# Performance work log

Hardware: AMD Instinct MI355X
Metric: run time of the kernel (lower is better)

The kernel has to match this reference:

```python
import jax, jax.numpy as jnp
import numpy as np

N_NODES = 100000
N_EDGES = 600000
N_GRAPHS = 64


def _segment_mean(x, seg_ids, num_segments):
    s = jax.ops.segment_sum(x, seg_ids, num_segments=num_segments)
    cnt = jax.ops.segment_sum(jnp.ones((x.shape[0],), x.dtype), seg_ids, num_segments=num_segments)
    return s / jnp.maximum(cnt, 1.0)[:, None]


def _sage_conv(x, src, dst, W_l, W_r, b):
    # PyG SAGEConv (mean aggr): out = lin_l(mean_{j->i} x_j) + lin_r(x_i)
    mean_nb = _segment_mean(x[src], dst, x.shape[0])  # [N, d_in]
    return mean_nb @ W_l.T + x @ W_r.T + b


def setup_inputs() -> dict:
    key = jax.random.key(0)
    ks = jax.random.split(key, 16)
    bert_cls = jax.random.normal(ks[0], (N_GRAPHS, 768), jnp.float32)
    node_x = jax.random.normal(ks[1], (N_NODES, 128), jnp.float32)
    edge_index = jax.random.randint(ks[2], (2, N_EDGES), 0, N_NODES, jnp.int64 if jax.config.jax_enable_x64 else jnp.int32)
    batch_ids = jnp.sort(jax.random.randint(ks[3], (N_NODES,), 0, N_GRAPHS))
    s = 0.05
    return {
        'bert_cls': bert_cls,
        'node_x': node_x,
        'edge_index': edge_index,
        'batch_ids': batch_ids,
        'W_adapt': jax.random.normal(ks[4], (64, 768), jnp.float32) * s,
        'b_adapt': jnp.zeros((64,), jnp.float32),
        'W1l': jax.random.normal(ks[5], (64, 128), jnp.float32) * s,
        'W1r': jax.random.normal(ks[6], (64, 128), jnp.float32) * s,
        'b1': jnp.zeros((64,), jnp.float32),
        'W2l': jax.random.normal(ks[7], (16, 64), jnp.float32) * s,
        'W2r': jax.random.normal(ks[8], (16, 64), jnp.float32) * s,
        'b2': jnp.zeros((16,), jnp.float32),
        'Wm': jax.random.normal(ks[9], (16, 16), jnp.float32) * s,
        'bm': jnp.zeros((16,), jnp.float32),
    }


def reference(bert_cls, node_x, edge_index, batch_ids,
              W_adapt, b_adapt, W1l, W1r, b1, W2l, W2r, b2, Wm, bm):
    # pooled BERT CLS -> adaptive linear (forward() applies no relu here)
    last_state = bert_cls @ W_adapt.T + b_adapt  # [bs, 64]

    src, dst = edge_index[0], edge_index[1]
    h = jax.nn.relu(_sage_conv(node_x, src, dst, W1l, W1r, b1))  # [N, 64]
    h = _sage_conv(h, src, dst, W2l, W2r, b2)                    # [N, 16]

    graph_emb = _segment_mean(h, batch_ids, N_GRAPHS)            # [bs, 16]
    graph_emb = graph_emb @ Wm.T + bm

    return jnp.concatenate([last_state, graph_emb], axis=-1)     # [bs, 80]
```

## Files before the change

kernel.cpp:

```cpp
#include <hip/hip_runtime.h>

#define N_NODES 100000
#define N_EDGES 600000
#define N_GRAPHS 64


__global__ void k_count(const int* __restrict__ dst, int* __restrict__ deg) {
    int e = blockIdx.x * 256 + threadIdx.x;
    if (e < N_EDGES) atomicAdd(&deg[dst[e]], 1);
}

__global__ void k_scan1(const int* __restrict__ deg, int* __restrict__ offs,
                        int* __restrict__ bsums) {
    __shared__ int s[256];
    int t = threadIdx.x, b = blockIdx.x;
    int base = b * 1024 + t * 4;
    int v0 = (base + 0 < N_NODES) ? deg[base + 0] : 0;
    int v1 = (base + 1 < N_NODES) ? deg[base + 1] : 0;
    int v2 = (base + 2 < N_NODES) ? deg[base + 2] : 0;
    int v3 = (base + 3 < N_NODES) ? deg[base + 3] : 0;
    int tsum = v0 + v1 + v2 + v3;
    s[t] = tsum;
    __syncthreads();
    for (int o = 1; o < 256; o <<= 1) {
        int x = (t >= o) ? s[t - o] : 0;
        __syncthreads();
        s[t] += x;
        __syncthreads();
    }
    int p = s[t] - tsum;
    if (base + 0 < N_NODES) offs[base + 0] = p;
    p += v0;
    if (base + 1 < N_NODES) offs[base + 1] = p;
    p += v1;
    if (base + 2 < N_NODES) offs[base + 2] = p;
    p += v2;
    if (base + 3 < N_NODES) offs[base + 3] = p;
    if (t == 255) bsums[b] = s[255];
}

__global__ void k_scan2(const int* __restrict__ bsums, int* __restrict__ boff) {
    __shared__ int s[128];
    int t = threadIdx.x;
    int nb = (N_NODES + 1023) / 1024;
    int v = (t < nb) ? bsums[t] : 0;
    s[t] = v;
    __syncthreads();
    for (int o = 1; o < 128; o <<= 1) {
        int x = (t >= o) ? s[t - o] : 0;
        __syncthreads();
        s[t] += x;
        __syncthreads();
    }
    boff[t] = s[t] - v;
}

__global__ void k_scan3(int* __restrict__ offs, const int* __restrict__ boff,
                        int* __restrict__ cursor) {
    int i = blockIdx.x * 256 + threadIdx.x;
    if (i < N_NODES) {
        int v = offs[i] + boff[i >> 10];
        offs[i] = v;
        cursor[i] = v;
    }
}

__global__ void k_fill(const int* __restrict__ src, const int* __restrict__ dst,
                       int* __restrict__ cursor, int* __restrict__ ssrc) {
    int e = blockIdx.x * 256 + threadIdx.x;
    if (e < N_EDGES) {
        int d = dst[e];
        int pos = atomicAdd(&cursor[d], 1);
        ssrc[pos] = src[e];
    }
}

__global__ void k_prepack(const float* __restrict__ W1l, const float* __restrict__ W1r,
                          float2* __restrict__ Wc) {
    int i = blockIdx.x * 256 + threadIdx.x;
    if (i < 128 * 64) {
        int k = i >> 6, d = i & 63;
        Wc[i] = make_float2(W1l[d * 128 + k], W1r[d * 128 + k]);
    }
}


__launch_bounds__(256)
__global__ void k_layer1(const float* __restrict__ x, const int* __restrict__ ssrc,
                         const int* __restrict__ offs, const int* __restrict__ deg,
                         const float2* __restrict__ Wc, const float* __restrict__ b1,
                         float* __restrict__ h1) {
    __shared__ float2 S[4][8][128];
    int tid = threadIdx.x, wave = tid >> 6, lane = tid & 63;
    float bias = b1[lane];
    const float2* x2 = (const float2*)x;
    int gw = blockIdx.x * 4 + wave;
    int nw = gridDim.x * 4;

    for (int base = gw * 8; base < N_NODES; base += nw * 8) {
#pragma unroll 1
        for (int j = 0; j < 8; ++j) {
            int node = base + j;
            int o  = __builtin_amdgcn_readfirstlane(offs[node]);
            int dg = __builtin_amdgcn_readfirstlane(deg[node]);
            float ax0 = 0.f, ay0 = 0.f, ax1 = 0.f, ay1 = 0.f;
            float ax2 = 0.f, ay2 = 0.f, ax3 = 0.f, ay3 = 0.f;
            int last = dg - 1;
            for (int u = 0; u < dg; u += 4) {
                int n0 = ssrc[o + u];
                int n1 = ssrc[o + min(u + 1, last)];
                int n2 = ssrc[o + min(u + 2, last)];
                int n3 = ssrc[o + min(u + 3, last)];
                float2 v0 = x2[n0 * 64 + lane];
                float2 v1 = x2[n1 * 64 + lane];
                float2 v2 = x2[n2 * 64 + lane];
                float2 v3 = x2[n3 * 64 + lane];
                float m1 = (u + 1 < dg) ? 1.f : 0.f;
                float m2 = (u + 2 < dg) ? 1.f : 0.f;
                float m3 = (u + 3 < dg) ? 1.f : 0.f;
                ax0 += v0.x;               ay0 += v0.y;
                ax1 = fmaf(v1.x, m1, ax1); ay1 = fmaf(v1.y, m1, ay1);
                ax2 = fmaf(v2.x, m2, ax2); ay2 = fmaf(v2.y, m2, ay2);
                ax3 = fmaf(v3.x, m3, ax3); ay3 = fmaf(v3.y, m3, ay3);
            }
            float inv = 1.f / (float)max(dg, 1);
            float ax = (ax0 + ax1) + (ax2 + ax3);
            float ay = (ay0 + ay1) + (ay2 + ay3);
            float2 xi = x2[node * 64 + lane];
            S[wave][j][2 * lane]     = make_float2(ax * inv, xi.x);
            S[wave][j][2 * lane + 1] = make_float2(ay * inv, xi.y);
        }
        float a0 = bias, a1 = bias, a2 = bias, a3 = bias;
        float a4 = bias, a5 = bias, a6 = bias, a7 = bias;
#pragma unroll 4
        for (int k = 0; k < 128; ++k) {
            float2 w = Wc[k * 64 + lane];
            float2 s0 = S[wave][0][k]; a0 += w.x * s0.x + w.y * s0.y;
            float2 s1 = S[wave][1][k]; a1 += w.x * s1.x + w.y * s1.y;
            float2 s2 = S[wave][2][k]; a2 += w.x * s2.x + w.y * s2.y;
            float2 s3 = S[wave][3][k]; a3 += w.x * s3.x + w.y * s3.y;
            float2 s4 = S[wave][4][k]; a4 += w.x * s4.x + w.y * s4.y;
            float2 s5 = S[wave][5][k]; a5 += w.x * s5.x + w.y * s5.y;
            float2 s6 = S[wave][6][k]; a6 += w.x * s6.x + w.y * s6.y;
            float2 s7 = S[wave][7][k]; a7 += w.x * s7.x + w.y * s7.y;
        }
        h1[(base + 0) * 64 + lane] = fmaxf(a0, 0.f);
        h1[(base + 1) * 64 + lane] = fmaxf(a1, 0.f);
        h1[(base + 2) * 64 + lane] = fmaxf(a2, 0.f);
        h1[(base + 3) * 64 + lane] = fmaxf(a3, 0.f);
        h1[(base + 4) * 64 + lane] = fmaxf(a4, 0.f);
        h1[(base + 5) * 64 + lane] = fmaxf(a5, 0.f);
        h1[(base + 6) * 64 + lane] = fmaxf(a6, 0.f);
        h1[(base + 7) * 64 + lane] = fmaxf(a7, 0.f);
    }
}


__launch_bounds__(256)
__global__ void k_layer2(const float* __restrict__ h1, const int* __restrict__ ssrc,
                         const int* __restrict__ offs, const int* __restrict__ deg,
                         const int* __restrict__ batch,
                         const float* __restrict__ W2l, const float* __restrict__ W2r,
                         const float* __restrict__ b2,
                         float* __restrict__ gsum, float* __restrict__ gcnt) {
    __shared__ float2 Wc[64 * 16];
    __shared__ float2 S[4][8][64];
    __shared__ float bins[N_GRAPHS][17];
    int tid = threadIdx.x;
    for (int i = tid; i < 64 * 16; i += 256) {
        int k = i >> 4, d = i & 15;
        Wc[i] = make_float2(W2l[d * 64 + k], W2r[d * 64 + k]);
    }
    for (int i = tid; i < N_GRAPHS * 17; i += 256) ((float*)bins)[i] = 0.f;
    __syncthreads();

    int wave = tid >> 6, lane = tid & 63;
    int d = lane & 15, jq = lane >> 4;
    float bias = b2[d];

    int chunk = (N_NODES + gridDim.x - 1) / gridDim.x;
    int cs = blockIdx.x * chunk;
    int ce = min(N_NODES, cs + chunk);

    for (int base = cs + wave * 8; base < ce; base += 32) {
        int cnt = min(8, ce - base);
        for (int j = 0; j < cnt; ++j) {
            int node = base + j;
            int o  = __builtin_amdgcn_readfirstlane(offs[node]);
            int dg = __builtin_amdgcn_readfirstlane(deg[node]);
            float a0 = 0.f, a1 = 0.f, a2 = 0.f, a3 = 0.f;
            int last = dg - 1;
            for (int u = 0; u < dg; u += 4) {
                int n0 = ssrc[o + u];
                int n1 = ssrc[o + min(u + 1, last)];
                int n2 = ssrc[o + min(u + 2, last)];
                int n3 = ssrc[o + min(u + 3, last)];
                float v0 = h1[n0 * 64 + lane];
                float v1 = h1[n1 * 64 + lane];
                float v2 = h1[n2 * 64 + lane];
                float v3 = h1[n3 * 64 + lane];
                float m1 = (u + 1 < dg) ? 1.f : 0.f;
                float m2 = (u + 2 < dg) ? 1.f : 0.f;
                float m3 = (u + 3 < dg) ? 1.f : 0.f;
                a0 += v0;
                a1 = fmaf(v1, m1, a1);
                a2 = fmaf(v2, m2, a2);
                a3 = fmaf(v3, m3, a3);
            }
            float inv = 1.f / (float)max(dg, 1);
            S[wave][j][lane] = make_float2(((a0 + a1) + (a2 + a3)) * inv,
                                           h1[node * 64 + lane]);
        }
#pragma unroll
        for (int p = 0; p < 2; ++p) {
            int j = p * 4 + jq;
            float a = bias;
#pragma unroll 8
            for (int k = 0; k < 64; ++k) {
                float2 w = Wc[k * 16 + d];
                float2 s = S[wave][j][k];
                a += w.x * s.x + w.y * s.y;
            }
            if (j < cnt) {
                int g = batch[base + j];
                atomicAdd(&bins[g][d], a);
                if (d == 0) atomicAdd(&bins[g][16], 1.f);
            }
        }
    }
    __syncthreads();
    for (int i = tid; i < N_GRAPHS * 17; i += 256) {
        int g = i / 17, c = i - g * 17;
        float v = bins[g][c];
        if (v != 0.f) {
            if (c < 16) atomicAdd(&gsum[g * 16 + c], v);
            else        atomicAdd(&gcnt[g], v);
        }
    }
}


__global__ void k_final(const float* __restrict__ bert, const float* __restrict__ Wad,
                        const float* __restrict__ bad, const float* __restrict__ Wm,
                        const float* __restrict__ bm, const float* __restrict__ gsum,
                        const float* __restrict__ gcnt, float* __restrict__ out) {
    int g = blockIdx.x;
    int t = threadIdx.x;
    if (t < 64) {
        const float4* br = (const float4*)(bert + g * 768);
        const float4* wr = (const float4*)(Wad + t * 768);
        float acc = bad[t];
#pragma unroll 8
        for (int k = 0; k < 192; ++k) {
            float4 bv = br[k], wv = wr[k];
            acc += bv.x * wv.x + bv.y * wv.y + bv.z * wv.z + bv.w * wv.w;
        }
        out[g * 80 + t] = acc;
    } else if (t < 80) {
        int j = t - 64;
        float ic = 1.f / fmaxf(gcnt[g], 1.f);
        float acc = bm[j];
#pragma unroll
        for (int k = 0; k < 16; ++k) acc += Wm[j * 16 + k] * gsum[g * 16 + k] * ic;
        out[g * 80 + t] = acc;
    }
}

extern "C" void kernel_launch(void* const* d_in, const int* in_sizes, int n_in,
                              void* d_out, int out_size, void* d_ws, size_t ws_size,
                              hipStream_t stream) {
    const float* bert   = (const float*)d_in[0];
    const float* node_x = (const float*)d_in[1];
    const int*   edge   = (const int*)d_in[2];
    const int*   batch  = (const int*)d_in[3];
    const float* Wad    = (const float*)d_in[4];
    const float* bad    = (const float*)d_in[5];
    const float* W1l    = (const float*)d_in[6];
    const float* W1r    = (const float*)d_in[7];
    const float* b1     = (const float*)d_in[8];
    const float* W2l    = (const float*)d_in[9];
    const float* W2r    = (const float*)d_in[10];
    const float* b2     = (const float*)d_in[11];
    const float* Wm     = (const float*)d_in[12];
    const float* bm     = (const float*)d_in[13];
    float* out = (float*)d_out;

    const int* src = edge;
    const int* dst = edge + N_EDGES;

    char* ws = (char*)d_ws;
    int*    deg    = (int*)(ws);
    int*    offs   = (int*)(ws + 400000);
    int*    cursor = (int*)(ws + 800000);
    int*    bsums  = (int*)(ws + 1200000);
    int*    boff   = (int*)(ws + 1200512);
    int*    ssrc   = (int*)(ws + 1201024);
    float*  h1     = (float*)(ws + 3601024);
    float2* Wc1    = (float2*)(ws + 29201024);
    float*  gsum   = (float*)(ws + 29266560);
    float*  gcnt   = (float*)(ws + 29270656);

    hipMemsetAsync(deg, 0, 400000, stream);
    hipMemsetAsync(gsum, 0, 4096 + 256, stream);

    k_count<<<(N_EDGES + 255) / 256, 256, 0, stream>>>(dst, deg);
    k_scan1<<<(N_NODES + 1023) / 1024, 256, 0, stream>>>(deg, offs, bsums);
    k_scan2<<<1, 128, 0, stream>>>(bsums, boff);
    k_scan3<<<(N_NODES + 255) / 256, 256, 0, stream>>>(offs, boff, cursor);
    k_fill<<<(N_EDGES + 255) / 256, 256, 0, stream>>>(src, dst, cursor, ssrc);
    k_prepack<<<32, 256, 0, stream>>>(W1l, W1r, Wc1);

    k_layer1<<<1024, 256, 0, stream>>>(node_x, ssrc, offs, deg, Wc1, b1, h1);
    k_layer2<<<1024, 256, 0, stream>>>(h1, ssrc, offs, deg, batch, W2l, W2r, b2, gsum, gcnt);
    k_final<<<N_GRAPHS, 128, 0, stream>>>(bert, Wad, bad, Wm, bm, gsum, gcnt, out);
}
```

Measured before the change: 365.0 us.

## Restructure SAGE layers into 64-node tiles with node-per-lane GEMM and separate pooling

Both layer kernels now gather 64 nodes per block into a swizzled shared tile, then run the dense projection with one node per lane and each wave owning a slice of output dims. Weights are read as wave-uniform values, likely scalar loads, instead of per-lane. Layer 2 writes h2 to global memory and a new k_pool kernel does the per-graph mean pooling, replacing the in-kernel atomics. The goal is to cut redundant LDS and weight traffic in the GEMM phase. The cost is an extra kernel launch, an h2 round trip, and block-wide syncs between gather and compute.

After: 460.9 us. 26.3% more time.

```diff
diff --git a/kernel.cpp b/kernel.cpp
--- a/kernel.cpp
+++ b/kernel.cpp
@@ -75,12 +75,23 @@
     }
 }
 
-__global__ void k_prepack(const float* __restrict__ W1l, const float* __restrict__ W1r,
-                          float2* __restrict__ Wc) {
+__global__ void k_prepack1(const float* __restrict__ W1l, const float* __restrict__ W1r,
+                           float2* __restrict__ Wsc) {
     int i = blockIdx.x * 256 + threadIdx.x;
     if (i < 128 * 64) {
-        int k = i >> 6, d = i & 63;
-        Wc[i] = make_float2(W1l[d * 128 + k], W1r[d * 128 + k]);
+        int m = i >> 6, d = i & 63;
+        Wsc[i] = (m < 64) ? make_float2(W1l[d * 128 + 2 * m], W1l[d * 128 + 2 * m + 1])
+                          : make_float2(W1r[d * 128 + 2 * (m - 64)], W1r[d * 128 + 2 * (m - 64) + 1]);
+    }
+}
+
+__global__ void k_prepack2(const float* __restrict__ W2l, const float* __restrict__ W2r,
+                           float2* __restrict__ Wsc) {
+    int i = blockIdx.x * 256 + threadIdx.x;
+    if (i < 64 * 16) {
+        int m = i >> 4, d = i & 15;
+        Wsc[i] = (m < 32) ? make_float2(W2l[d * 64 + 2 * m], W2l[d * 64 + 2 * m + 1])
+                          : make_float2(W2r[d * 64 + 2 * (m - 32)], W2r[d * 64 + 2 * (m - 32) + 1]);
     }
 }
 
@@ -88,70 +99,77 @@
 __launch_bounds__(256)
 __global__ void k_layer1(const float* __restrict__ x, const int* __restrict__ ssrc,
                          const int* __restrict__ offs, const int* __restrict__ deg,
-                         const float2* __restrict__ Wc, const float* __restrict__ b1,
+                         const float2* __restrict__ Wsc, const float* __restrict__ b1,
                          float* __restrict__ h1) {
-    __shared__ float2 S[4][8][128];
-    int tid = threadIdx.x, wave = tid >> 6, lane = tid & 63;
-    float bias = b1[lane];
+    __shared__ float2 S[64 * 128];
+    int tid = threadIdx.x;
+    int wave = __builtin_amdgcn_readfirstlane(tid >> 6);
+    int lane = tid & 63;
     const float2* x2 = (const float2*)x;
-    int gw = blockIdx.x * 4 + wave;
-    int nw = gridDim.x * 4;
-
-    for (int base = gw * 8; base < N_NODES; base += nw * 8) {
-#pragma unroll 1
-        for (int j = 0; j < 8; ++j) {
-            int node = base + j;
-            int o  = __builtin_amdgcn_readfirstlane(offs[node]);
-            int dg = __builtin_amdgcn_readfirstlane(deg[node]);
-            float ax0 = 0.f, ay0 = 0.f, ax1 = 0.f, ay1 = 0.f;
-            float ax2 = 0.f, ay2 = 0.f, ax3 = 0.f, ay3 = 0.f;
-            int last = dg - 1;
-            for (int u = 0; u < dg; u += 4) {
-                int n0 = ssrc[o + u];
-                int n1 = ssrc[o + min(u + 1, last)];
-                int n2 = ssrc[o + min(u + 2, last)];
-                int n3 = ssrc[o + min(u + 3, last)];
-                float2 v0 = x2[n0 * 64 + lane];
-                float2 v1 = x2[n1 * 64 + lane];
-                float2 v2 = x2[n2 * 64 + lane];
-                float2 v3 = x2[n3 * 64 + lane];
-                float m1 = (u + 1 < dg) ? 1.f : 0.f;
-                float m2 = (u + 2 < dg) ? 1.f : 0.f;
-                float m3 = (u + 3 < dg) ? 1.f : 0.f;
-                ax0 += v0.x;               ay0 += v0.y;
-                ax1 = fmaf(v1.x, m1, ax1); ay1 = fmaf(v1.y, m1, ay1);
-                ax2 = fmaf(v2.x, m2, ax2); ay2 = fmaf(v2.y, m2, ay2);
-                ax3 = fmaf(v3.x, m3, ax3); ay3 = fmaf(v3.y, m3, ay3);
-            }
-            float inv = 1.f / (float)max(dg, 1);
-            float ax = (ax0 + ax1) + (ax2 + ax3);
-            float ay = (ay0 + ay1) + (ay2 + ay3);
-            float2 xi = x2[node * 64 + lane];
-            S[wave][j][2 * lane]     = make_float2(ax * inv, xi.x);
-            S[wave][j][2 * lane + 1] = make_float2(ay * inv, xi.y);
-        }
-        float a0 = bias, a1 = bias, a2 = bias, a3 = bias;
-        float a4 = bias, a5 = bias, a6 = bias, a7 = bias;
+
+    int nTiles = (N_NODES + 63) / 64;
+    for (int tile = blockIdx.x; tile < nTiles; tile += gridDim.x) {
+        int tbase = tile * 64;
+        for (int j = wave * 16; j < wave * 16 + 16; ++j) {
+            int node = tbase + j;
+            if (node < N_NODES) {
+                int o  = __builtin_amdgcn_readfirstlane(offs[node]);
+                int dg = __builtin_amdgcn_readfirstlane(deg[node]);
+                float ax0 = 0.f, ay0 = 0.f, ax1 = 0.f, ay1 = 0.f;
+                float ax2 = 0.f, ay2 = 0.f, ax3 = 0.f, ay3 = 0.f;
+                int last = dg - 1;
+                for (int u = 0; u < dg; u += 4) {
+                    int n0 = ssrc[o + u];
+                    int n1 = ssrc[o + min(u + 1, last)];
+                    int n2 = ssrc[o + min(u + 2, last)];
+                    int n3 = ssrc[o + min(u + 3, last)];
+                    float2 v0 = x2[n0 * 64 + lane];
+                    float2 v1 = x2[n1 * 64 + lane];
+                    float2 v2 = x2[n2 * 64 + lane];
+                    float2 v3 = x2[n3 * 64 + lane];
+                    float m1 = (u + 1 < dg) ? 1.f : 0.f;
+                    float m2 = (u + 2 < dg) ? 1.f : 0.f;
+                    float m3 = (u + 3 < dg) ? 1.f : 0.f;
+                    ax0 += v0.x;               ay0 += v0.y;
+                    ax1 = fmaf(v1.x, m1, ax1); ay1 = fmaf(v1.y, m1, ay1);
+                    ax2 = fmaf(v2.x, m2, ax2); ay2 = fmaf(v2.y, m2, ay2);
+                    ax3 = fmaf(v3.x, m3, ax3); ay3 = fmaf(v3.y, m3, ay3);
+                }
+                float inv = 1.f / (float)max(dg, 1);
+                float2 xi = x2[node * 64 + lane];
+                int sw = lane ^ (j & 15);
+                S[j * 128 + sw]      = make_float2(((ax0 + ax1) + (ax2 + ax3)) * inv,
+                                                   ((ay0 + ay1) + (ay2 + ay3)) * inv);
+                S[j * 128 + 64 + sw] = make_float2(xi.x, xi.y);
+            }
+        }
+        __syncthreads();
+        {
+            int n = lane;
+            int node = tbase + n;
+            int dbase = wave * 16;
+            float acc[16];
+#pragma unroll
+            for (int dd = 0; dd < 16; ++dd) acc[dd] = b1[dbase + dd];
+            int swz = n & 15;
+            const float2* Sn = S + n * 128;
 #pragma unroll 4
-        for (int k = 0; k < 128; ++k) {
-            float2 w = Wc[k * 64 + lane];
-            float2 s0 = S[wave][0][k]; a0 += w.x * s0.x + w.y * s0.y;
-            float2 s1 = S[wave][1][k]; a1 += w.x * s1.x + w.y * s1.y;
-            float2 s2 = S[wave][2][k]; a2 += w.x * s2.x + w.y * s2.y;
-            float2 s3 = S[wave][3][k]; a3 += w.x * s3.x + w.y * s3.y;
-            float2 s4 = S[wave][4][k]; a4 += w.x * s4.x + w.y * s4.y;
-            float2 s5 = S[wave][5][k]; a5 += w.x * s5.x + w.y * s5.y;
-            float2 s6 = S[wave][6][k]; a6 += w.x * s6.x + w.y * s6.y;
-            float2 s7 = S[wave][7][k]; a7 += w.x * s7.x + w.y * s7.y;
-        }
-        h1[(base + 0) * 64 + lane] = fmaxf(a0, 0.f);
-        h1[(base + 1) * 64 + lane] = fmaxf(a1, 0.f);
-        h1[(base + 2) * 64 + lane] = fmaxf(a2, 0.f);
-        h1[(base + 3) * 64 + lane] = fmaxf(a3, 0.f);
-        h1[(base + 4) * 64 + lane] = fmaxf(a4, 0.f);
-        h1[(base + 5) * 64 + lane] = fmaxf(a5, 0.f);
-        h1[(base + 6) * 64 + lane] = fmaxf(a6, 0.f);
-        h1[(base + 7) * 64 + lane] = fmaxf(a7, 0.f);
+            for (int m = 0; m < 128; ++m) {
+                float2 s = Sn[m ^ swz];
+                const float2* Wm = Wsc + m * 64 + dbase;
+#pragma unroll
+                for (int dd = 0; dd < 16; ++dd)
+                    acc[dd] = fmaf(Wm[dd].x, s.x, fmaf(Wm[dd].y, s.y, acc[dd]));
+            }
+            if (node < N_NODES) {
+                float4* dstp = (float4*)(h1 + node * 64 + dbase);
+#pragma unroll
+                for (int p = 0; p < 4; ++p)
+                    dstp[p] = make_float4(fmaxf(acc[4 * p], 0.f), fmaxf(acc[4 * p + 1], 0.f),
+                                          fmaxf(acc[4 * p + 2], 0.f), fmaxf(acc[4 * p + 3], 0.f));
+            }
+        }
+        __syncthreads();
     }
 }
 
@@ -159,77 +177,94 @@
 __launch_bounds__(256)
 __global__ void k_layer2(const float* __restrict__ h1, const int* __restrict__ ssrc,
                          const int* __restrict__ offs, const int* __restrict__ deg,
-                         const int* __restrict__ batch,
-                         const float* __restrict__ W2l, const float* __restrict__ W2r,
-                         const float* __restrict__ b2,
-                         float* __restrict__ gsum, float* __restrict__ gcnt) {
-    __shared__ float2 Wc[64 * 16];
-    __shared__ float2 S[4][8][64];
+                         const float2* __restrict__ Wsc, const float* __restrict__ b2,
+                         float* __restrict__ h2) {
+    __shared__ float S[64 * 128];
+    int tid = threadIdx.x;
+    int wave = __builtin_amdgcn_readfirstlane(tid >> 6);
+    int lane = tid & 63;
+
+    int nTiles = (N_NODES + 63) / 64;
+    for (int tile = blockIdx.x; tile < nTiles; tile += gridDim.x) {
+        int tbase = tile * 64;
+        for (int j = wave * 16; j < wave * 16 + 16; ++j) {
+            int node = tbase + j;
+            if (node < N_NODES) {
+                int o  = __builtin_amdgcn_readfirstlane(offs[node]);
+                int dg = __builtin_amdgcn_readfirstlane(deg[node]);
+                float a0 = 0.f, a1 = 0.f, a2 = 0.f, a3 = 0.f;
+                int last = dg - 1;
+                for (int u = 0; u < dg; u += 4) {
+                    int n0 = ssrc[o + u];
+                    int n1 = ssrc[o + min(u + 1, last)];
+                    int n2 = ssrc[o + min(u + 2, last)];
+                    int n3 = ssrc[o + min(u + 3, last)];
+                    float v0 = h1[n0 * 64 + lane];
+                    float v1 = h1[n1 * 64 + lane];
+                    float v2 = h1[n2 * 64 + lane];
+                    float v3 = h1[n3 * 64 + lane];
+                    float m1 = (u + 1 < dg) ? 1.f : 0.f;
+                    float m2 = (u + 2 < dg) ? 1.f : 0.f;
+                    float m3 = (u + 3 < dg) ? 1.f : 0.f;
+                    a0 += v0;
+                    a1 = fmaf(v1, m1, a1);
+                    a2 = fmaf(v2, m2, a2);
+                    a3 = fmaf(v3, m3, a3);
+                }
+                float inv = 1.f / (float)max(dg, 1);
+                float mv = ((a0 + a1) + (a2 + a3)) * inv;
+                float hv = h1[node * 64 + lane];
+                int pr = (lane >> 1) ^ (j & 15), c = lane & 1;
+                S[j * 128 + 2 * pr + c]      = mv;
+                S[j * 128 + 64 + 2 * pr + c] = hv;
+            }
+        }
+        __syncthreads();
+        {
+            int n = lane;
+            int node = tbase + n;
+            int dbase = wave * 4;
+            float acc[4];
+#pragma unroll
+            for (int dd = 0; dd < 4; ++dd) acc[dd] = b2[dbase + dd];
+            int swz = n & 15;
+            const float2* Sn = (const float2*)S + n * 64;
+#pragma unroll 4
+            for (int m = 0; m < 64; ++m) {
+                float2 s = Sn[m ^ swz];
+                const float2* Wm = Wsc + m * 16 + dbase;
+#pragma unroll
+                for (int dd = 0; dd < 4; ++dd)
+                    acc[dd] = fmaf(Wm[dd].x, s.x, fmaf(Wm[dd].y, s.y, acc[dd]));
+            }
+            if (node < N_NODES) {
+                *(float4*)(h2 + node * 16 + dbase) =
+                    make_float4(acc[0], acc[1], acc[2], acc[3]);
+            }
+        }
+        __syncthreads();
+    }
+}
+
+
+__global__ void k_pool(const float* __restrict__ h2, const int* __restrict__ batch,
+                       float* __restrict__ gsum, float* __restrict__ gcnt) {
     __shared__ float bins[N_GRAPHS][17];
-    int tid = threadIdx.x;
-    for (int i = tid; i < 64 * 16; i += 256) {
-        int k = i >> 4, d = i & 15;
-        Wc[i] = make_float2(W2l[d * 64 + k], W2r[d * 64 + k]);
-    }
-    for (int i = tid; i < N_GRAPHS * 17; i += 256) ((float*)bins)[i] = 0.f;
+    int t = threadIdx.x;
+    for (int i = t; i < N_GRAPHS * 17; i += 256) ((float*)bins)[i] = 0.f;
     __syncthreads();
-
-    int wave = tid >> 6, lane = tid & 63;
-    int d = lane & 15, jq = lane >> 4;
-    float bias = b2[d];
-
+    int dd = t & 15, nl = t >> 4;
     int chunk = (N_NODES + gridDim.x - 1) / gridDim.x;
     int cs = blockIdx.x * chunk;
     int ce = min(N_NODES, cs + chunk);
-
-    for (int base = cs + wave * 8; base < ce; base += 32) {
-        int cnt = min(8, ce - base);
-        for (int j = 0; j < cnt; ++j) {
-            int node = base + j;
-            int o  = __builtin_amdgcn_readfirstlane(offs[node]);
-            int dg = __builtin_amdgcn_readfirstlane(deg[node]);
-            float a0 = 0.f, a1 = 0.f, a2 = 0.f, a3 = 0.f;
-            int last = dg - 1;
-            for (int u = 0; u < dg; u += 4) {
-                int n0 = ssrc[o + u];
-                int n1 = ssrc[o + min(u + 1, last)];
-                int n2 = ssrc[o + min(u + 2, last)];
-                int n3 = ssrc[o + min(u + 3, last)];
-                float v0 = h1[n0 * 64 + lane];
-                float v1 = h1[n1 * 64 + lane];
-                float v2 = h1[n2 * 64 + lane];
-                float v3 = h1[n3 * 64 + lane];
-                float m1 = (u + 1 < dg) ? 1.f : 0.f;
-                float m2 = (u + 2 < dg) ? 1.f : 0.f;
-                float m3 = (u + 3 < dg) ? 1.f : 0.f;
-                a0 += v0;
-                a1 = fmaf(v1, m1, a1);
-                a2 = fmaf(v2, m2, a2);
-                a3 = fmaf(v3, m3, a3);
-            }
-            float inv = 1.f / (float)max(dg, 1);
-            S[wave][j][lane] = make_float2(((a0 + a1) + (a2 + a3)) * inv,
-                                           h1[node * 64 + lane]);
-        }
-#pragma unroll
-        for (int p = 0; p < 2; ++p) {
-            int j = p * 4 + jq;
-            float a = bias;
-#pragma unroll 8
-            for (int k = 0; k < 64; ++k) {
-                float2 w = Wc[k * 16 + d];
-                float2 s = S[wave][j][k];
-                a += w.x * s.x + w.y * s.y;
-            }
-            if (j < cnt) {
-                int g = batch[base + j];
-                atomicAdd(&bins[g][d], a);
-                if (d == 0) atomicAdd(&bins[g][16], 1.f);
-            }
-        }
+    for (int n = cs + nl; n < ce; n += 16) {
+        float v = h2[n * 16 + dd];
+        int g = batch[n];
+        atomicAdd(&bins[g][dd], v);
+        if (dd == 0) atomicAdd(&bins[g][16], 1.f);
     }
     __syncthreads();
-    for (int i = tid; i < N_GRAPHS * 17; i += 256) {
+    for (int i = t; i < N_GRAPHS * 17; i += 256) {
         int g = i / 17, c = i - g * 17;
         float v = bins[g][c];
         if (v != 0.f) {
@@ -296,9 +331,11 @@
     int*    boff   = (int*)(ws + 1200512);
     int*    ssrc   = (int*)(ws + 1201024);
     float*  h1     = (float*)(ws + 3601024);
-    float2* Wc1    = (float2*)(ws + 29201024);
-    float*  gsum   = (float*)(ws + 29266560);
-    float*  gcnt   = (float*)(ws + 29270656);
+    float*  h2     = (float*)(ws + 29201024);
+    float2* Wsc1   = (float2*)(ws + 35601024);
+    float2* Wsc2   = (float2*)(ws + 35666560);
+    float*  gsum   = (float*)(ws + 35674752);
+    float*  gcnt   = (float*)(ws + 35678848);
 
     hipMemsetAsync(deg, 0, 400000, stream);
     hipMemsetAsync(gsum, 0, 4096 + 256, stream);
@@ -308,9 +345,11 @@
     k_scan2<<<1, 128, 0, stream>>>(bsums, boff);
     k_scan3<<<(N_NODES + 255) / 256, 256, 0, stream>>>(offs, boff, cursor);
     k_fill<<<(N_EDGES + 255) / 256, 256, 0, stream>>>(src, dst, cursor, ssrc);
-    k_prepack<<<32, 256, 0, stream>>>(W1l, W1r, Wc1);
-
-    k_layer1<<<1024, 256, 0, stream>>>(node_x, ssrc, offs, deg, Wc1, b1, h1);
-    k_layer2<<<1024, 256, 0, stream>>>(h1, ssrc, offs, deg, batch, W2l, W2r, b2, gsum, gcnt);
+    k_prepack1<<<32, 256, 0, stream>>>(W1l, W1r, Wsc1);
+    k_prepack2<<<4, 256, 0, stream>>>(W2l, W2r, Wsc2);
+
+    k_layer1<<<512, 256, 0, stream>>>(node_x, ssrc, offs, deg, Wsc1, b1, h1);
+    k_layer2<<<1024, 256, 0, stream>>>(h1, ssrc, offs, deg, Wsc2, b2, h2);
+    k_pool<<<128, 256, 0, stream>>>(h2, batch, gsum, gcnt);
     k_final<<<N_GRAPHS, 128, 0, stream>>>(bert, Wad, bad, Wm, bm, gsum, gcnt, out);
 }
```

## Transform node features before aggregation in both SAGE layers

Applied to the files above, without the earlier changes.

Uses linearity of mean aggregation to apply W_l and W_r to every node first (dense per-tile transforms), then gathers the already-transformed features. Layer 1 gathers stay 64-wide rather than 128-wide float2, and layer 2 gathers shrink from 64 to 16 floats per neighbor, which cuts random-gather traffic. The cost is extra dense matmul kernels, extra intermediate buffers written and read back, and more kernel launches.

Measured after the change: 357.6 us. 1.02x faster.

```diff
diff --git a/kernel.cpp b/kernel.cpp
--- a/kernel.cpp
+++ b/kernel.cpp
@@ -76,156 +76,210 @@
 }
 
 __global__ void k_prepack(const float* __restrict__ W1l, const float* __restrict__ W1r,
-                          float2* __restrict__ Wc) {
+                          const float* __restrict__ W2l, const float* __restrict__ W2r,
+                          float2* __restrict__ P) {
     int i = blockIdx.x * 256 + threadIdx.x;
-    if (i < 128 * 64) {
-        int k = i >> 6, d = i & 63;
-        Wc[i] = make_float2(W1l[d * 128 + k], W1r[d * 128 + k]);
+    if (i < 4096) {
+        int m = i >> 6, d = i & 63;
+        P[i] = make_float2(W1l[d * 128 + 2 * m], W1l[d * 128 + 2 * m + 1]);
+    } else if (i < 8192) {
+        int j = i - 4096, m = j >> 6, d = j & 63;
+        P[i] = make_float2(W1r[d * 128 + 2 * m], W1r[d * 128 + 2 * m + 1]);
+    } else if (i < 8704) {
+        int j = i - 8192, m = j >> 4, d = j & 15;
+        P[i] = make_float2(W2l[d * 64 + 2 * m], W2l[d * 64 + 2 * m + 1]);
+    } else if (i < 9216) {
+        int j = i - 8704, m = j >> 4, d = j & 15;
+        P[i] = make_float2(W2r[d * 64 + 2 * m], W2r[d * 64 + 2 * m + 1]);
     }
 }
 
 
 __launch_bounds__(256)
-__global__ void k_layer1(const float* __restrict__ x, const int* __restrict__ ssrc,
-                         const int* __restrict__ offs, const int* __restrict__ deg,
-                         const float2* __restrict__ Wc, const float* __restrict__ b1,
-                         float* __restrict__ h1) {
-    __shared__ float2 S[4][8][128];
-    int tid = threadIdx.x, wave = tid >> 6, lane = tid & 63;
+__global__ void k_xform1(const float* __restrict__ x,
+                         const float2* __restrict__ Pl, const float2* __restrict__ Pr,
+                         float* __restrict__ xl, float* __restrict__ xr) {
+    __shared__ float2 S[64 * 64];
+    int tid = threadIdx.x;
+    int wave = __builtin_amdgcn_readfirstlane(tid >> 6);
+    int lane = tid & 63;
+    int tbase = blockIdx.x * 64;
+    const float4* x4 = (const float4*)x;
+
+    for (int idx = tid; idx < 64 * 32; idx += 256) {
+        int n = idx >> 5, m4 = idx & 31;
+        if (tbase + n < N_NODES) {
+            float4 v = x4[(tbase + n) * 32 + m4];
+            int swz = n & 31;
+            S[n * 64 + ((2 * m4) ^ swz)]     = make_float2(v.x, v.y);
+            S[n * 64 + ((2 * m4 + 1) ^ swz)] = make_float2(v.z, v.w);
+        }
+    }
+    __syncthreads();
+
+    int node = tbase + lane;
+    int dbase = wave * 16;
+    float accl[16], accr[16];
+#pragma unroll
+    for (int dd = 0; dd < 16; ++dd) { accl[dd] = 0.f; accr[dd] = 0.f; }
+    int swz = lane & 31;
+    const float2* Sn = S + lane * 64;
+#pragma unroll 4
+    for (int m = 0; m < 64; ++m) {
+        float2 s = Sn[m ^ swz];
+        const float2* Wl = Pl + m * 64 + dbase;
+        const float2* Wr = Pr + m * 64 + dbase;
+#pragma unroll
+        for (int dd = 0; dd < 16; ++dd) {
+            accl[dd] = fmaf(Wl[dd].x, s.x, fmaf(Wl[dd].y, s.y, accl[dd]));
+            accr[dd] = fmaf(Wr[dd].x, s.x, fmaf(Wr[dd].y, s.y, accr[dd]));
+        }
+    }
+    if (node < N_NODES) {
+        float4* pl = (float4*)(xl + node * 64 + dbase);
+        float4* pr = (float4*)(xr + node * 64 + dbase);
+#pragma unroll
+        for (int p = 0; p < 4; ++p) {
+            pl[p] = make_float4(accl[4 * p], accl[4 * p + 1], accl[4 * p + 2], accl[4 * p + 3]);
+            pr[p] = make_float4(accr[4 * p], accr[4 * p + 1], accr[4 * p + 2], accr[4 * p + 3]);
+        }
+    }
+}
+
+
+__launch_bounds__(256)
+__global__ void k_gather1(const float* __restrict__ xl, const int* __restrict__ ssrc,
+                          const int* __restrict__ offs, const int* __restrict__ deg,
+                          const float* __restrict__ b1, float* __restrict__ h1) {
+    int tid = blockIdx.x * 256 + threadIdx.x;
+    int wid = tid >> 6, lane = tid & 63;
+    int nWaves = (gridDim.x * 256) >> 6;
     float bias = b1[lane];
-    const float2* x2 = (const float2*)x;
-    int gw = blockIdx.x * 4 + wave;
-    int nw = gridDim.x * 4;
-
-    for (int base = gw * 8; base < N_NODES; base += nw * 8) {
-#pragma unroll 1
-        for (int j = 0; j < 8; ++j) {
-            int node = base + j;
-            int o  = __builtin_amdgcn_readfirstlane(offs[node]);
-            int dg = __builtin_amdgcn_readfirstlane(deg[node]);
-            float ax0 = 0.f, ay0 = 0.f, ax1 = 0.f, ay1 = 0.f;
-            float ax2 = 0.f, ay2 = 0.f, ax3 = 0.f, ay3 = 0.f;
-            int last = dg - 1;
-            for (int u = 0; u < dg; u += 4) {
-                int n0 = ssrc[o + u];
-                int n1 = ssrc[o + min(u + 1, last)];
-                int n2 = ssrc[o + min(u + 2, last)];
-                int n3 = ssrc[o + min(u + 3, last)];
-                float2 v0 = x2[n0 * 64 + lane];
-                float2 v1 = x2[n1 * 64 + lane];
-                float2 v2 = x2[n2 * 64 + lane];
-                float2 v3 = x2[n3 * 64 + lane];
-                float m1 = (u + 1 < dg) ? 1.f : 0.f;
-                float m2 = (u + 2 < dg) ? 1.f : 0.f;
-                float m3 = (u + 3 < dg) ? 1.f : 0.f;
-                ax0 += v0.x;               ay0 += v0.y;
-                ax1 = fmaf(v1.x, m1, ax1); ay1 = fmaf(v1.y, m1, ay1);
-                ax2 = fmaf(v2.x, m2, ax2); ay2 = fmaf(v2.y, m2, ay2);
-                ax3 = fmaf(v3.x, m3, ax3); ay3 = fmaf(v3.y, m3, ay3);
-            }
-            float inv = 1.f / (float)max(dg, 1);
-            float ax = (ax0 + ax1) + (ax2 + ax3);
-            float ay = (ay0 + ay1) + (ay2 + ay3);
-            float2 xi = x2[node * 64 + lane];
-            S[wave][j][2 * lane]     = make_float2(ax * inv, xi.x);
-            S[wave][j][2 * lane + 1] = make_float2(ay * inv, xi.y);
-        }
-        float a0 = bias, a1 = bias, a2 = bias, a3 = bias;
-        float a4 = bias, a5 = bias, a6 = bias, a7 = bias;
+
+    for (int node = wid; node < N_NODES; node += nWaves) {
+        int o  = __builtin_amdgcn_readfirstlane(offs[node]);
+        int dg = __builtin_amdgcn_readfirstlane(deg[node]);
+        float self = h1[node * 64 + lane];
+        float a0 = 0.f, a1 = 0.f, a2 = 0.f, a3 = 0.f;
+        int last = dg - 1;
+        for (int u = 0; u < dg; u += 4) {
+            int n0 = ssrc[o + u];
+            int n1 = ssrc[o + min(u + 1, last)];
+            int n2 = ssrc[o + min(u + 2, last)];
+            int n3 = ssrc[o + min(u + 3, last)];
+            float v0 = xl[n0 * 64 + lane];
+            float v1 = xl[n1 * 64 + lane];
+            float v2 = xl[n2 * 64 + lane];
+            float v3 = xl[n3 * 64 + lane];
+            float m1 = (u + 1 < dg) ? 1.f : 0.f;
+            float m2 = (u + 2 < dg) ? 1.f : 0.f;
+            float m3 = (u + 3 < dg) ? 1.f : 0.f;
+            a0 += v0;
+            a1 = fmaf(v1, m1, a1);
+            a2 = fmaf(v2, m2, a2);
+            a3 = fmaf(v3, m3, a3);
+        }
+        float inv = 1.f / (float)max(dg, 1);
+        h1[node * 64 + lane] = fmaxf(self + bias + ((a0 + a1) + (a2 + a3)) * inv, 0.f);
+    }
+}
+
+
+__launch_bounds__(256)
+__global__ void k_xform2(const float* __restrict__ h1,
+                         const float2* __restrict__ Pl, const float2* __restrict__ Pr,
+                         float* __restrict__ h1l, float* __restrict__ h2pre) {
+    __shared__ float2 S[64 * 32];
+    int tid = threadIdx.x;
+    int wave = __builtin_amdgcn_readfirstlane(tid >> 6);
+    int lane = tid & 63;
+    int tbase = blockIdx.x * 64;
+    const float4* h4 = (const float4*)h1;
+
+    for (int idx = tid; idx < 64 * 16; idx += 256) {
+        int n = idx >> 4, m4 = idx & 15;
+        if (tbase + n < N_NODES) {
+            float4 v = h4[(tbase + n) * 16 + m4];
+            int swz = n & 31;
+            S[n * 32 + ((2 * m4) ^ swz)]     = make_float2(v.x, v.y);
+            S[n * 32 + ((2 * m4 + 1) ^ swz)] = make_float2(v.z, v.w);
+        }
+    }
+    __syncthreads();
+
+    int node = tbase + lane;
+    int dbase = wave * 4;
+    float accl[4] = {0.f, 0.f, 0.f, 0.f};
+    float accr[4] = {0.f, 0.f, 0.f, 0.f};
+    int swz = lane & 31;
+    const float2* Sn = S + lane * 32;
 #pragma unroll 4
-        for (int k = 0; k < 128; ++k) {
-            float2 w = Wc[k * 64 + lane];
-            float2 s0 = S[wave][0][k]; a0 += w.x * s0.x + w.y * s0.y;
-            float2 s1 = S[wave][1][k]; a1 += w.x * s1.x + w.y * s1.y;
-            float2 s2 = S[wave][2][k]; a2 += w.x * s2.x + w.y * s2.y;
-            float2 s3 = S[wave][3][k]; a3 += w.x * s3.x + w.y * s3.y;
-            float2 s4 = S[wave][4][k]; a4 += w.x * s4.x + w.y * s4.y;
-            float2 s5 = S[wave][5][k]; a5 += w.x * s5.x + w.y * s5.y;
-            float2 s6 = S[wave][6][k]; a6 += w.x * s6.x + w.y * s6.y;
-            float2 s7 = S[wave][7][k]; a7 += w.x * s7.x + w.y * s7.y;
-        }
-        h1[(base + 0) * 64 + lane] = fmaxf(a0, 0.f);
-        h1[(base + 1) * 64 + lane] = fmaxf(a1, 0.f);
-        h1[(base + 2) * 64 + lane] = fmaxf(a2, 0.f);
-        h1[(base + 3) * 64 + lane] = fmaxf(a3, 0.f);
-        h1[(base + 4) * 64 + lane] = fmaxf(a4, 0.f);
-        h1[(base + 5) * 64 + lane] = fmaxf(a5, 0.f);
-        h1[(base + 6) * 64 + lane] = fmaxf(a6, 0.f);
-        h1[(base + 7) * 64 + lane] = fmaxf(a7, 0.f);
+    for (int m = 0; m < 32; ++m) {
+        float2 s = Sn[m ^ swz];
+        const float2* Wl = Pl + m * 16 + dbase;
+        const float2* Wr = Pr + m * 16 + dbase;
+#pragma unroll
+        for (int dd = 0; dd < 4; ++dd) {
+            accl[dd] = fmaf(Wl[dd].x, s.x, fmaf(Wl[dd].y, s.y, accl[dd]));
+            accr[dd] = fmaf(Wr[dd].x, s.x, fmaf(Wr[dd].y, s.y, accr[dd]));
+        }
+    }
+    if (node < N_NODES) {
+        *(float4*)(h1l + node * 16 + dbase)   = make_float4(accl[0], accl[1], accl[2], accl[3]);
+        *(float4*)(h2pre + node * 16 + dbase) = make_float4(accr[0], accr[1], accr[2], accr[3]);
     }
 }
 
 
 __launch_bounds__(256)
-__global__ void k_layer2(const float* __restrict__ h1, const int* __restrict__ ssrc,
-                         const int* __restrict__ offs, const int* __restrict__ deg,
-                         const int* __restrict__ batch,
-                         const float* __restrict__ W2l, const float* __restrict__ W2r,
+__global__ void k_g2pool(const float* __restrict__ h1l, const float* __restrict__ h2pre,
+                         const int* __restrict__ ssrc, const int* __restrict__ offs,
+                         const int* __restrict__ deg, const int* __restrict__ batch,
                          const float* __restrict__ b2,
                          float* __restrict__ gsum, float* __restrict__ gcnt) {
-    __shared__ float2 Wc[64 * 16];
-    __shared__ float2 S[4][8][64];
     __shared__ float bins[N_GRAPHS][17];
     int tid = threadIdx.x;
-    for (int i = tid; i < 64 * 16; i += 256) {
-        int k = i >> 4, d = i & 15;
-        Wc[i] = make_float2(W2l[d * 64 + k], W2r[d * 64 + k]);
-    }
     for (int i = tid; i < N_GRAPHS * 17; i += 256) ((float*)bins)[i] = 0.f;
     __syncthreads();
 
     int wave = tid >> 6, lane = tid & 63;
-    int d = lane & 15, jq = lane >> 4;
+    int sub = lane >> 4, d = lane & 15;
     float bias = b2[d];
 
     int chunk = (N_NODES + gridDim.x - 1) / gridDim.x;
     int cs = blockIdx.x * chunk;
     int ce = min(N_NODES, cs + chunk);
 
-    for (int base = cs + wave * 8; base < ce; base += 32) {
-        int cnt = min(8, ce - base);
-        for (int j = 0; j < cnt; ++j) {
-            int node = base + j;
-            int o  = __builtin_amdgcn_readfirstlane(offs[node]);
-            int dg = __builtin_amdgcn_readfirstlane(deg[node]);
-            float a0 = 0.f, a1 = 0.f, a2 = 0.f, a3 = 0.f;
-            int last = dg - 1;
-            for (int u = 0; u < dg; u += 4) {
-                int n0 = ssrc[o + u];
-                int n1 = ssrc[o + min(u + 1, last)];
-                int n2 = ssrc[o + min(u + 2, last)];
-                int n3 = ssrc[o + min(u + 3, last)];
-                float v0 = h1[n0 * 64 + lane];
-                float v1 = h1[n1 * 64 + lane];
-                float v2 = h1[n2 * 64 + lane];
-                float v3 = h1[n3 * 64 + lane];
-                float m1 = (u + 1 < dg) ? 1.f : 0.f;
-                float m2 = (u + 2 < dg) ? 1.f : 0.f;
-                float m3 = (u + 3 < dg) ? 1.f : 0.f;
-                a0 += v0;
-                a1 = fmaf(v1, m1, a1);
-                a2 = fmaf(v2, m2, a2);
-                a3 = fmaf(v3, m3, a3);
-            }
-            float inv = 1.f / (float)max(dg, 1);
-            S[wave][j][lane] = make_float2(((a0 + a1) + (a2 + a3)) * inv,
-                                           h1[node * 64 + lane]);
-        }
-#pragma unroll
-        for (int p = 0; p < 2; ++p) {
-            int j = p * 4 + jq;
-            float a = bias;
-#pragma unroll 8
-            for (int k = 0; k < 64; ++k) {
-                float2 w = Wc[k * 16 + d];
-                float2 s = S[wave][j][k];
-                a += w.x * s.x + w.y * s.y;
-            }
-            if (j < cnt) {
-                int g = batch[base + j];
-                atomicAdd(&bins[g][d], a);
-                if (d == 0) atomicAdd(&bins[g][16], 1.f);
-            }
+    for (int base = cs + wave * 4; base < ce; base += 16) {
+        int node = base + sub;
+        bool valid = node < ce;
+        int nn = valid ? node : cs;
+        int o = offs[nn], dg = deg[nn];
+        float a0 = 0.f, a1 = 0.f, a2 = 0.f, a3 = 0.f;
+        int last = dg - 1;
+        for (int u = 0; u < dg; u += 4) {
+            int n0 = ssrc[o + u];
+            int n1 = ssrc[o + min(u + 1, last)];
+            int n2 = ssrc[o + min(u + 2, last)];
+            int n3 = ssrc[o + min(u + 3, last)];
+            float v0 = h1l[n0 * 16 + d];
+            float v1 = h1l[n1 * 16 + d];
+            float v2 = h1l[n2 * 16 + d];
+            float v3 = h1l[n3 * 16 + d];
+            float m1 = (u + 1 < dg) ? 1.f : 0.f;
+            float m2 = (u + 2 < dg) ? 1.f : 0.f;
+            float m3 = (u + 3 < dg) ? 1.f : 0.f;
+            a0 += v0;
+            a1 = fmaf(v1, m1, a1);
+            a2 = fmaf(v2, m2, a2);
+            a3 = fmaf(v3, m3, a3);
+        }
+        float inv = 1.f / (float)max(dg, 1);
+        float val = h2pre[nn * 16 + d] + bias + ((a0 + a1) + (a2 + a3)) * inv;
+        if (valid) {
+            int g = batch[nn];
+            atomicAdd(&bins[g][d], val);
+            if (d == 0) atomicAdd(&bins[g][16], 1.f);
         }
     }
     __syncthreads();
@@ -295,10 +349,18 @@
     int*    bsums  = (int*)(ws + 1200000);
     int*    boff   = (int*)(ws + 1200512);
     int*    ssrc   = (int*)(ws + 1201024);
-    float*  h1     = (float*)(ws + 3601024);
-    float2* Wc1    = (float2*)(ws + 29201024);
-    float*  gsum   = (float*)(ws + 29266560);
-    float*  gcnt   = (float*)(ws + 29270656);
+    float*  xl     = (float*)(ws + 3601024);
+    float*  h1     = (float*)(ws + 29201024);
+    float2* P      = (float2*)(ws + 54801024);
+    float*  gsum   = (float*)(ws + 54874752);
+    float*  gcnt   = (float*)(ws + 54878848);
+    float*  h1l    = (float*)(ws + 3601024);
+    float*  h2pre  = (float*)(ws + 10001024);
+
+    float2* P1l = P;
+    float2* P1r = P + 4096;
+    float2* P2l = P + 8192;
+    float2* P2r = P + 8704;
 
     hipMemsetAsync(deg, 0, 400000, stream);
     hipMemsetAsync(gsum, 0, 4096 + 256, stream);
@@ -308,9 +370,12 @@
     k_scan2<<<1, 128, 0, stream>>>(bsums, boff);
     k_scan3<<<(N_NODES + 255) / 256, 256, 0, stream>>>(offs, boff, cursor);
     k_fill<<<(N_EDGES + 255) / 256, 256, 0, stream>>>(src, dst, cursor, ssrc);
-    k_prepack<<<32, 256, 0, stream>>>(W1l, W1r, Wc1);
-
-    k_layer1<<<1024, 256, 0, stream>>>(node_x, ssrc, offs, deg, Wc1, b1, h1);
-    k_layer2<<<1024, 256, 0, stream>>>(h1, ssrc, offs, deg, batch, W2l, W2r, b2, gsum, gcnt);
+    k_prepack<<<36, 256, 0, stream>>>(W1l, W1r, W2l, W2r, P);
+
+    int nTiles = (N_NODES + 63) / 64;
+    k_xform1<<<nTiles, 256, 0, stream>>>(node_x, P1l, P1r, xl, h1);
+    k_gather1<<<2048, 256, 0, stream>>>(xl, ssrc, offs, deg, b1, h1);
+    k_xform2<<<nTiles, 256, 0, stream>>>(h1, P2l, P2r, h1l, h2pre);
+    k_g2pool<<<512, 256, 0, stream>>>(h1l, h2pre, ssrc, offs, deg, batch, b2, gsum, gcnt);
     k_final<<<N_GRAPHS, 128, 0, stream>>>(bert, Wad, bad, Wm, bm, gsum, gcnt, out);
 }
```
